# Kernel optimization log

Measured on AMD Instinct MI355X. Metric: run time of the kernel, lower is better.

The kernel has to match this reference:

```python
import jax, jax.numpy as jnp
import numpy as np

B, T, DIM = 1, 4096, 768
H, D = 6, 128  # num_heads, head_dim
ATTN_SCALE = 0.12
EPS = 1.1920929e-07  # torch fp32 rms_norm default eps


def _rms_norm(x):
    # F.rms_norm over last dim, no learned weight
    return x * jax.lax.rsqrt(jnp.mean(jnp.square(x), axis=-1, keepdims=True) + EPS)


def _rotary_tables(seq_len, head_dim):
    # angular_freq: (1/1024)**linspace(0,1,D//4) concat zeros(D//4) -> length D//2
    af = (1.0 / 1024.0) ** jnp.linspace(0.0, 1.0, head_dim // 4, dtype=jnp.float32)
    af = jnp.concatenate([af, jnp.zeros(head_dim // 4, dtype=jnp.float32)])
    t = jnp.arange(seq_len, dtype=jnp.float32)
    theta = t[:, None] * af[None, :]  # [T, D//2]
    return jnp.cos(theta), jnp.sin(theta)


def _apply_rotary(x_bthd, cos, sin):
    # x: [B,T,H,D]; rotate pairs (x1, x2) = halves of last dim
    x1, x2 = jnp.split(x_bthd.astype(jnp.float32), 2, axis=-1)
    c = cos[None, :, None, :]
    s = sin[None, :, None, :]
    y1 = x1 * c + x2 * s
    y2 = -x1 * s + x2 * c
    return jnp.concatenate([y1, y2], axis=-1).astype(x_bthd.dtype)


def setup_inputs() -> dict:
    key = jax.random.key(0)
    k1, k2, k3, k4, k5 = jax.random.split(key, 5)
    std = 0.5 * DIM ** (-0.5)
    bound = (3.0 ** 0.5) * std
    x = jax.random.normal(k1, (B, T, DIM), dtype=jnp.float32)
    ve = jax.random.normal(k2, (B, T, DIM), dtype=jnp.float32)
    qkv_w = jax.random.uniform(k3, (3, H * D, DIM), dtype=jnp.float32, minval=-bound, maxval=bound)
    lambdas = jnp.array([0.5, 0.5], dtype=jnp.float32)
    # original zero-inits c_proj; use small random weights for a nontrivial output
    c_proj_w = jax.random.uniform(k5, (DIM, H * D), dtype=jnp.float32, minval=-bound, maxval=bound)
    return {"x": x, "ve": ve, "qkv_w": qkv_w, "lambdas": lambdas, "c_proj_w": c_proj_w}


def reference(x, ve, qkv_w, lambdas, c_proj_w):
    Bx, Tx = x.shape[0], x.shape[1]
    # fused QKV: linear with weight [3*hdim, dim] -> [B,T,3*H,D]
    qkv = jnp.einsum('btd,ehd->bteh', x, qkv_w.reshape(3 * H, D, DIM).reshape(3 * H * D, DIM).reshape(3 * H, D, DIM))
    # simpler: flatten weight and reshape output
    w_flat = qkv_w.reshape(3 * H * D, DIM)
    qkv = (x @ w_flat.T).reshape(Bx, Tx, 3 * H, D)
    q, k, v = jnp.split(qkv, 3, axis=2)  # each [B,T,H,D]
    q, k = _rms_norm(q), _rms_norm(k)
    cos, sin = _rotary_tables(Tx, D)
    q, k = _apply_rotary(q, cos, sin), _apply_rotary(k, cos, sin)
    v = lambdas[0] * v + lambdas[1] * ve.reshape(Bx, Tx, H, D)
    # causal attention with non-standard scale
    scores = jnp.einsum('bthd,bshd->bhts', q, k) * ATTN_SCALE  # [B,H,T,T]
    causal = jnp.tril(jnp.ones((Tx, Tx), dtype=bool))
    scores = jnp.where(causal[None, None], scores, -jnp.inf)
    probs = jax.nn.softmax(scores, axis=-1)
    y = jnp.einsum('bhts,bshd->bthd', probs, v).reshape(Bx, Tx, H * D)
    return y @ c_proj_w.T
```

## Files before the change

kernel.cpp:

```cpp
#include <hip/hip_runtime.h>
#include <hip/hip_bf16.h>

using bf16 = __hip_bfloat16;
typedef __attribute__((ext_vector_type(8))) __bf16 bf16x8;
typedef __attribute__((ext_vector_type(4))) float f32x4;

static constexpr int T = 4096, DIM = 768, H = 6, D = 128, N3 = 2304;
static constexpr int PPH = 280;
static constexpr float kEps = 1.1920929e-07f;
static constexpr float kC1 = 0.12f * 1.44269504f;
static constexpr float kTHR = 11.54f;

__device__ __forceinline__ void gll16(const bf16* g, bf16* l) {
  __builtin_amdgcn_global_load_lds((const __attribute__((address_space(1))) void*)g,
                                   (__attribute__((address_space(3))) void*)l, 16, 0, 0);
}

__device__ __forceinline__ int pre_qt(int qt) {
  const int k = qt >> 3, rr = qt & 7;
  return qt + 4 * k * (k - 1) + rr * k;
}

__global__ __launch_bounds__(256) void prep(const float* __restrict__ x,
                                            const float* __restrict__ qkv_w,
                                            const float* __restrict__ cproj,
                                            bf16* __restrict__ xb, bf16* __restrict__ wb,
                                            bf16* __restrict__ cb, float2* __restrict__ tab) {
  const int NBX = T * DIM / 2048, NBW = N3 * DIM / 2048, NBC = DIM * DIM / 2048;
  int b = blockIdx.x;
  const int tid = threadIdx.x;
  if (b < NBX + NBW + NBC) {
    const float* in;
    bf16* out;
    if (b < NBX) { in = x; out = xb; }
    else if (b < NBX + NBW) { in = qkv_w; out = wb; b -= NBX; }
    else { in = cproj; out = cb; b -= NBX + NBW; }
    const int i = (b * 256 + tid) * 8;
    const float4 a = *(const float4*)(in + i);
    const float4 c = *(const float4*)(in + i + 4);
    bf16 t[8] = {(bf16)a.x, (bf16)a.y, (bf16)a.z, (bf16)a.w,
                 (bf16)c.x, (bf16)c.y, (bf16)c.z, (bf16)c.w};
    *(int4*)(out + i) = *(const int4*)t;
  } else {
    b -= NBX + NBW + NBC;
    const int i = b * 256 + tid;
    const int t = i >> 5, j = i & 31;
    const float af = exp2f(-10.f * (float)j * (1.f / 31.f));
    float s, c;
    sincosf((float)t * af, &s, &c);
    tab[i] = make_float2(c, s);
  }
}

__global__ __launch_bounds__(256, 4) void gemm_qkv(const bf16* __restrict__ A,
                                                   const bf16* __restrict__ B,
                                                   const float2* __restrict__ tab,
                                                   const float* __restrict__ ve,
                                                   const float* __restrict__ lam,
                                                   bf16* __restrict__ qb,
                                                   bf16* __restrict__ kb,
                                                   bf16* __restrict__ vt) {
  __shared__ bf16 sh[12288];
  const int tid = threadIdx.x, lane = tid & 63, wid = tid >> 6;
  const int slice = blockIdx.x;
  const int brow = blockIdx.y * 64;
  const int bcol = slice * 128;
  const int wm = (wid >> 1) * 32, wn = (wid & 1) * 64;
  const int r = lane & 15, g = lane >> 4;
  f32x4 acc[2][4] = {};
  const int lrow = lane >> 3;
  const int scol = (lane & 7) * 8;
  const bf16* gA = A + (long)(brow + wid * 16 + lrow) * DIM + scol;
  const bf16* gB = B + (long)(bcol + wid * 32 + lrow) * DIM + scol;
  for (int k0 = 0; k0 < DIM; k0 += 64) {
    __syncthreads();
#pragma unroll
    for (int i = 0; i < 2; ++i)
      gll16(gA + (long)i * 8 * DIM + k0, sh + (wid * 16 + i * 8) * 64);
#pragma unroll
    for (int i = 0; i < 4; ++i)
      gll16(gB + (long)i * 8 * DIM + k0, sh + 4096 + (wid * 32 + i * 8) * 64);
    __syncthreads();
#pragma unroll
    for (int kk = 0; kk < 2; ++kk) {
      bf16x8 af[2], bfr[4];
#pragma unroll
      for (int m = 0; m < 2; ++m)
        af[m] = *(const bf16x8*)(sh + (wm + m * 16 + r) * 64 + kk * 32 + g * 8);
#pragma unroll
      for (int n = 0; n < 4; ++n)
        bfr[n] = *(const bf16x8*)(sh + 4096 + (wn + n * 16 + r) * 64 + kk * 32 + g * 8);
#pragma unroll
      for (int m = 0; m < 2; ++m)
#pragma unroll
        for (int n = 0; n < 4; ++n)
          acc[m][n] = __builtin_amdgcn_mfma_f32_16x16x32_bf16(af[m], bfr[n], acc[m][n], 0, 0, 0);
    }
  }
  __syncthreads();
#pragma unroll
  for (int m = 0; m < 2; ++m)
#pragma unroll
    for (int n = 0; n < 4; ++n)
#pragma unroll
      for (int q = 0; q < 4; ++q)
        sh[(wm + m * 16 + g * 4 + q) * 137 + wn + n * 16 + r] = (bf16)acc[m][n][q];
  __syncthreads();
  const int type = slice / 6, h = slice % 6;
  if (type < 2) {
    const int row = tid >> 2, p0 = (tid & 3) * 16;
    const int t = brow + row;
    float x1[16], x2[16];
    float ss = 0.f;
#pragma unroll
    for (int j = 0; j < 16; ++j) {
      x1[j] = __bfloat162float(sh[row * 137 + p0 + j]);
      x2[j] = __bfloat162float(sh[row * 137 + p0 + 64 + j]);
      ss += x1[j] * x1[j] + x2[j] * x2[j];
    }
    ss += __shfl_xor(ss, 1);
    ss += __shfl_xor(ss, 2);
    const float sc = rsqrtf(ss * (1.f / 128.f) + kEps) * (type == 0 ? kC1 : 1.f);
    bf16 y1[16], y2[16];
#pragma unroll
    for (int j = 0; j < 16; ++j) {
      float c = 1.f, s = 0.f;
      if (p0 + j < 32) { const float2 cs = tab[t * 32 + p0 + j]; c = cs.x; s = cs.y; }
      const float a = x1[j] * sc, b = x2[j] * sc;
      y1[j] = (bf16)(a * c + b * s);
      y2[j] = (bf16)(b * c - a * s);
    }
    bf16* dst = (type == 0 ? qb : kb) + ((long)h * T + t) * D + p0;
    *(int4*)(dst) = *(const int4*)&y1[0];
    *(int4*)(dst + 8) = *(const int4*)&y1[8];
    *(int4*)(dst + 64) = *(const int4*)&y2[0];
    *(int4*)(dst + 72) = *(const int4*)&y2[8];
  } else {
    const float l0 = lam[0], l1 = lam[1];
    const int row = tid >> 2, seg = (tid & 3) * 32;
    const float* vs = ve + (long)(brow + row) * DIM + h * D + seg;
#pragma unroll
    for (int j = 0; j < 32; j += 4) {
      const float4 e = *(const float4*)(vs + j);
      const float ef[4] = {e.x, e.y, e.z, e.w};
#pragma unroll
      for (int u = 0; u < 4; ++u) {
        const int c = seg + j + u;
        sh[row * 137 + c] = (bf16)(l0 * __bfloat162float(sh[row * 137 + c]) + l1 * ef[u]);
      }
    }
    __syncthreads();
    const int d = tid >> 1, half = tid & 1;
    bf16 outr[32];
#pragma unroll
    for (int j = 0; j < 32; ++j) outr[j] = sh[(half * 32 + j) * 137 + d];
    bf16* dst = vt + ((long)h * D + d) * T + brow + half * 32;
#pragma unroll
    for (int c = 0; c < 4; ++c)
      *(int4*)(dst + c * 8) = *(const int4*)&outr[c * 8];
  }
}

template <typename CT>
__global__ __launch_bounds__(256, 4) void gemm_bt(const bf16* __restrict__ A,
                                                  const bf16* __restrict__ B,
                                                  CT* __restrict__ C,
                                                  int M, int N, int K) {
  __shared__ bf16 lA[64][64];
  __shared__ bf16 lB[128][64];
  const int tid = threadIdx.x, lane = tid & 63, wid = tid >> 6;
  const int brow = blockIdx.y * 64, bcol = blockIdx.x * 128;
  const int wm = (wid >> 1) * 32, wn = (wid & 1) * 64;
  const int r = lane & 15, g = lane >> 4;
  f32x4 acc[2][4] = {};
  const int lrow = lane >> 3;
  const int scol = (lane & 7) * 8;
  const bf16* gA = A + (long)(brow + wid * 16 + lrow) * K + scol;
  const bf16* gB = B + (long)(bcol + wid * 32 + lrow) * K + scol;
  for (int k0 = 0; k0 < K; k0 += 64) {
    __syncthreads();
#pragma unroll
    for (int i = 0; i < 2; ++i)
      gll16(gA + (long)i * 8 * K + k0, &lA[wid * 16 + i * 8][0]);
#pragma unroll
    for (int i = 0; i < 4; ++i)
      gll16(gB + (long)i * 8 * K + k0, &lB[wid * 32 + i * 8][0]);
    __syncthreads();
#pragma unroll
    for (int kk = 0; kk < 2; ++kk) {
      bf16x8 af[2], bfr[4];
#pragma unroll
      for (int m = 0; m < 2; ++m)
        af[m] = *(const bf16x8*)&lA[wm + m * 16 + r][kk * 32 + g * 8];
#pragma unroll
      for (int n = 0; n < 4; ++n)
        bfr[n] = *(const bf16x8*)&lB[wn + n * 16 + r][kk * 32 + g * 8];
#pragma unroll
      for (int m = 0; m < 2; ++m)
#pragma unroll
        for (int n = 0; n < 4; ++n)
          acc[m][n] = __builtin_amdgcn_mfma_f32_16x16x32_bf16(af[m], bfr[n], acc[m][n], 0, 0, 0);
    }
  }
  const int crow = brow + wm + g * 4;
  const int ccol = bcol + wn + r;
#pragma unroll
  for (int m = 0; m < 2; ++m)
#pragma unroll
    for (int n = 0; n < 4; ++n)
#pragma unroll
      for (int q = 0; q < 4; ++q)
        C[(long)(crow + m * 16 + q) * N + ccol + n * 16] = (CT)acc[m][n][q];
}

__global__ __launch_bounds__(512, 4) void attn(const bf16* __restrict__ qb,
                                               const bf16* __restrict__ kb,
                                               const bf16* __restrict__ vt,
                                               bf16* __restrict__ po,
                                               float* __restrict__ pm,
                                               float* __restrict__ ps,
                                               bf16* __restrict__ yb) {
  __shared__ bf16 Kl[64][128];
  __shared__ bf16 Vl[128][64];
  __shared__ bf16 Pl[8][16][64];
  const int bid = blockIdx.x;
  const int h = bid % H;
  const int fi = bid / H;
  int s = 31, ci = 0, acc0 = 0;
  for (int ss = 31; ss >= 0; --ss) {
    const int n = (ss >> 2) + 1;
    if (fi < acc0 + n) { s = ss; ci = fi - acc0; break; }
    acc0 += n;
  }
  const int tid = threadIdx.x, lane = tid & 63, w = tid >> 6;
  const int r = lane & 15, g = lane >> 4;
  const int qt = 2 * s + (w >> 2);
  const int wrow = (w & 3) * 16;
  const int ts = ci * 8;
  const int te = min(ts + 8, 2 * s + 2);

  bf16x8 qf[4];
#pragma unroll
  for (int kk = 0; kk < 4; ++kk)
    qf[kk] = *(const bf16x8*)(qb + ((long)h * T + qt * 64 + wrow + r) * D + kk * 32 + g * 8);
  f32x4 o[8] = {};
  float m[4], sl[4];
#pragma unroll
  for (int q = 0; q < 4; ++q) { m[q] = -1e30f; sl[q] = 0.f; }

  auto STAGE = [&](int t) {
    const int kv0 = t * 64;
#pragma unroll
    for (int i = 0; i < 2; ++i) {
      const int seg = w * 2 + i;
      {
        const int lr = seg * 4 + (lane >> 4);
        const int cs = (lane & 15) ^ (lr & 7);
        gll16(kb + ((long)h * T + kv0 + lr) * D + cs * 8,
              (bf16*)&Kl[0][0] + seg * 512);
      }
      {
        const int lr = seg * 8 + (lane >> 3);
        const int cs = (lane & 7) ^ (lr & 7);
        gll16(vt + ((long)h * D + lr) * T + kv0 + cs * 8,
              (bf16*)&Vl[0][0] + seg * 512);
      }
    }
  };

  STAGE(ts);
  __syncthreads();
  for (int tt = ts; tt < te; ++tt) {
    const bool act = (tt <= qt);
    if (act) {
      const bf16* Kb = (const bf16*)&Kl[0][0];
      const bf16* Vb = (const bf16*)&Vl[0][0];
      bf16* Pb = &Pl[w][0][0];
      f32x4 st4[4];
      __builtin_amdgcn_s_setprio(1);
#pragma unroll
      for (int stt = 0; stt < 4; ++stt) {
        f32x4 a = {};
        const int lrk = stt * 16 + r;
#pragma unroll
        for (int kk = 0; kk < 4; ++kk) {
          const bf16x8 kf = *(const bf16x8*)(Kb + lrk * 128 + (((kk * 4 + g) ^ (lrk & 7)) * 8));
          a = __builtin_amdgcn_mfma_f32_16x16x32_bf16(qf[kk], kf, a, 0, 0, 0);
        }
        st4[stt] = a;
      }
      __builtin_amdgcn_s_setprio(0);
      if (tt == qt) {
        const int qgl = qt * 64 + wrow + 4 * g;
#pragma unroll
        for (int stt = 0; stt < 4; ++stt)
#pragma unroll
          for (int q = 0; q < 4; ++q)
            if (tt * 64 + stt * 16 + r > qgl + q) st4[stt][q] = -1e30f;
      }
      float mx[4];
#pragma unroll
      for (int q = 0; q < 4; ++q)
        mx[q] = fmaxf(fmaxf(st4[0][q], st4[1][q]), fmaxf(st4[2][q], st4[3][q]));
      const float dd = fmaxf(fmaxf(mx[0] - m[0], mx[1] - m[1]),
                             fmaxf(mx[2] - m[2], mx[3] - m[3]));
      if (__any(dd > kTHR)) {
#pragma unroll
        for (int off = 1; off < 16; off <<= 1)
#pragma unroll
          for (int q = 0; q < 4; ++q) mx[q] = fmaxf(mx[q], __shfl_xor(mx[q], off));
#pragma unroll
        for (int q = 0; q < 4; ++q) {
          const float nm = fmaxf(m[q], mx[q]);
          const float al = exp2f(m[q] - nm);
          m[q] = nm;
          sl[q] *= al;
#pragma unroll
          for (int nn = 0; nn < 8; ++nn) o[nn][q] *= al;
        }
      }
#pragma unroll
      for (int stt = 0; stt < 4; ++stt)
#pragma unroll
        for (int q = 0; q < 4; ++q)
          st4[stt][q] = exp2f(st4[stt][q] - m[q]);
#pragma unroll
      for (int q = 0; q < 4; ++q)
        sl[q] += (st4[0][q] + st4[1][q]) + (st4[2][q] + st4[3][q]);
#pragma unroll
      for (int stt = 0; stt < 4; ++stt)
#pragma unroll
        for (int q = 0; q < 4; ++q) {
          const int rw = 4 * g + q;
          Pb[rw * 64 + ((stt * 16 + r) ^ ((rw & 7) << 3))] = (bf16)st4[stt][q];
        }
      bf16x8 pf[2];
#pragma unroll
      for (int kk = 0; kk < 2; ++kk)
        pf[kk] = *(const bf16x8*)(Pb + r * 64 + (((kk * 4 + g) ^ (r & 7)) * 8));
      __builtin_amdgcn_s_setprio(1);
#pragma unroll
      for (int nn = 0; nn < 8; ++nn) {
        const int d = nn * 16 + r;
#pragma unroll
        for (int kk = 0; kk < 2; ++kk) {
          const bf16x8 vf = *(const bf16x8*)(Vb + d * 64 + (((kk * 4 + g) ^ (d & 7)) * 8));
          o[nn] = __builtin_amdgcn_mfma_f32_16x16x32_bf16(pf[kk], vf, o[nn], 0, 0, 0);
        }
      }
      __builtin_amdgcn_s_setprio(0);
    }
    if (tt + 1 < te) {
      __syncthreads();
      STAGE(tt + 1);
      __syncthreads();
    }
  }
#pragma unroll
  for (int off = 1; off < 16; off <<= 1)
#pragma unroll
    for (int q = 0; q < 4; ++q) sl[q] += __shfl_xor(sl[q], off);
  const int row0 = wrow + 4 * g;
  if (s < 4) {
#pragma unroll
    for (int nn = 0; nn < 8; ++nn)
#pragma unroll
      for (int q = 0; q < 4; ++q)
        yb[(long)(qt * 64 + row0 + q) * DIM + h * D + nn * 16 + r] = (bf16)(o[nn][q] / sl[q]);
  } else {
    const long part = (long)h * PPH + (pre_qt(qt) - 8) + ci;
    bf16* pob = po + part * 8192;
#pragma unroll
    for (int nn = 0; nn < 8; ++nn)
#pragma unroll
      for (int q = 0; q < 4; ++q)
        pob[(row0 + q) * 128 + nn * 16 + r] = (bf16)o[nn][q];
    if (r == 0) {
#pragma unroll
      for (int q = 0; q < 4; ++q) {
        pm[part * 64 + row0 + q] = m[q];
        ps[part * 64 + row0 + q] = sl[q];
      }
    }
  }
}

__global__ __launch_bounds__(256) void attn_reduce(const bf16* __restrict__ po,
                                                   const float* __restrict__ pm,
                                                   const float* __restrict__ ps,
                                                   bf16* __restrict__ yb) {
  const int qt = 8 + blockIdx.x, h = blockIdx.y;
  const int tid = threadIdx.x;
  const int row = tid >> 2, seg = (tid & 3) * 32;
  const int nch = (qt >> 3) + 1;
  const long base = (long)h * PPH + pre_qt(qt) - 8;
  float mm = -1e30f;
  for (int ci = 0; ci < nch; ++ci) mm = fmaxf(mm, pm[(base + ci) * 64 + row]);
  float den = 0.f;
  for (int ci = 0; ci < nch; ++ci)
    den += ps[(base + ci) * 64 + row] * exp2f(pm[(base + ci) * 64 + row] - mm);
  const float inv = 1.f / den;
  float acc[32] = {};
  for (int ci = 0; ci < nch; ++ci) {
    const float wq = exp2f(pm[(base + ci) * 64 + row] - mm) * inv;
    const bf16* src = po + (base + ci) * 8192 + row * 128 + seg;
#pragma unroll
    for (int j = 0; j < 32; j += 8) {
      const bf16x8 v = *(const bf16x8*)(src + j);
#pragma unroll
      for (int u = 0; u < 8; ++u) acc[j + u] += wq * (float)v[u];
    }
  }
  bf16 outv[32];
#pragma unroll
  for (int j = 0; j < 32; ++j) outv[j] = (bf16)acc[j];
  bf16* dst = yb + (long)(qt * 64 + row) * DIM + h * D + seg;
#pragma unroll
  for (int cc = 0; cc < 4; ++cc)
    *(int4*)(dst + cc * 8) = *(const int4*)&outv[cc * 8];
}

extern "C" void kernel_launch(void* const* d_in, const int* in_sizes, int n_in,
                              void* d_out, int out_size, void* d_ws, size_t ws_size,
                              hipStream_t stream) {
  const float* x     = (const float*)d_in[0];
  const float* ve    = (const float*)d_in[1];
  const float* qkv_w = (const float*)d_in[2];
  const float* lam   = (const float*)d_in[3];
  const float* cproj = (const float*)d_in[4];
  float* out = (float*)d_out;

  bf16* cb  = (bf16*)d_ws;
  bf16* qb  = cb + (long)DIM * DIM;
  bf16* kb  = qb + (long)H * T * D;
  bf16* vt  = kb + (long)H * T * D;
  bf16* yb  = vt + (long)H * T * D;
  float2* tab = (float2*)(yb + (long)T * DIM);
  bf16* xb  = (bf16*)(tab + (long)T * 32);
  bf16* wb  = xb + (long)T * DIM;
  bf16* po  = xb;
  float* pm = (float*)(po + (long)PPH * H * 8192);
  float* ps = pm + (long)PPH * H * 64;

  const int NBX = T * DIM / 2048, NBW = N3 * DIM / 2048, NBC = DIM * DIM / 2048;
  prep<<<dim3(NBX + NBW + NBC + T * 32 / 256), 256, 0, stream>>>(x, qkv_w, cproj, xb, wb, cb, tab);

  gemm_qkv<<<dim3(N3 / 128, T / 64), 256, 0, stream>>>(xb, wb, tab, ve, lam, qb, kb, vt);
  attn<<<dim3(144 * H), 512, 0, stream>>>(qb, kb, vt, po, pm, ps, yb);
  attn_reduce<<<dim3(56, H), 256, 0, stream>>>(po, pm, ps, yb);
  gemm_bt<float><<<dim3(DIM / 128, T / 64), 256, 0, stream>>>(yb, cb, out, T, DIM, DIM);
}
```

Before: 134.8 us.

## Double-buffer attention K/V tiles at 32-key granularity and shrink output GEMM tiles

The attention kernel now stages K/V in 32-key tiles across two LDS buffers, prefetching the next tile before computing the current one. This replaces the previous pattern of two barriers around each synchronous 64-key load, so global loads can overlap MFMA work. The split work per block keeps the same key span (16 half-tiles), and the causal mask and active checks are adjusted for the finer granularity. Separately, the output projection GEMM uses 64x64 tiles instead of 64x128, which doubles the number of blocks and helps the small problem fill the GPU. The smaller K-steps mean more loop iterations and more per-tile softmax overhead.

Measured after the change: 131.9 us. 2.2% less time.

```diff
diff --git a/kernel.cpp b/kernel.cpp
--- a/kernel.cpp
+++ b/kernel.cpp
@@ -167,38 +167,37 @@
                                                   CT* __restrict__ C,
                                                   int M, int N, int K) {
   __shared__ bf16 lA[64][64];
-  __shared__ bf16 lB[128][64];
+  __shared__ bf16 lB[64][64];
   const int tid = threadIdx.x, lane = tid & 63, wid = tid >> 6;
-  const int brow = blockIdx.y * 64, bcol = blockIdx.x * 128;
-  const int wm = (wid >> 1) * 32, wn = (wid & 1) * 64;
+  const int brow = blockIdx.y * 64, bcol = blockIdx.x * 64;
+  const int wm = (wid >> 1) * 32, wn = (wid & 1) * 32;
   const int r = lane & 15, g = lane >> 4;
-  f32x4 acc[2][4] = {};
+  f32x4 acc[2][2] = {};
   const int lrow = lane >> 3;
   const int scol = (lane & 7) * 8;
   const bf16* gA = A + (long)(brow + wid * 16 + lrow) * K + scol;
-  const bf16* gB = B + (long)(bcol + wid * 32 + lrow) * K + scol;
+  const bf16* gB = B + (long)(bcol + wid * 16 + lrow) * K + scol;
   for (int k0 = 0; k0 < K; k0 += 64) {
     __syncthreads();
 #pragma unroll
-    for (int i = 0; i < 2; ++i)
+    for (int i = 0; i < 2; ++i) {
       gll16(gA + (long)i * 8 * K + k0, &lA[wid * 16 + i * 8][0]);
-#pragma unroll
-    for (int i = 0; i < 4; ++i)
-      gll16(gB + (long)i * 8 * K + k0, &lB[wid * 32 + i * 8][0]);
+      gll16(gB + (long)i * 8 * K + k0, &lB[wid * 16 + i * 8][0]);
+    }
     __syncthreads();
 #pragma unroll
     for (int kk = 0; kk < 2; ++kk) {
-      bf16x8 af[2], bfr[4];
+      bf16x8 af[2], bfr[2];
 #pragma unroll
       for (int m = 0; m < 2; ++m)
         af[m] = *(const bf16x8*)&lA[wm + m * 16 + r][kk * 32 + g * 8];
 #pragma unroll
-      for (int n = 0; n < 4; ++n)
+      for (int n = 0; n < 2; ++n)
         bfr[n] = *(const bf16x8*)&lB[wn + n * 16 + r][kk * 32 + g * 8];
 #pragma unroll
       for (int m = 0; m < 2; ++m)
 #pragma unroll
-        for (int n = 0; n < 4; ++n)
+        for (int n = 0; n < 2; ++n)
           acc[m][n] = __builtin_amdgcn_mfma_f32_16x16x32_bf16(af[m], bfr[n], acc[m][n], 0, 0, 0);
     }
   }
@@ -207,7 +206,7 @@
 #pragma unroll
   for (int m = 0; m < 2; ++m)
 #pragma unroll
-    for (int n = 0; n < 4; ++n)
+    for (int n = 0; n < 2; ++n)
 #pragma unroll
       for (int q = 0; q < 4; ++q)
         C[(long)(crow + m * 16 + q) * N + ccol + n * 16] = (CT)acc[m][n][q];
@@ -220,9 +219,9 @@
                                                float* __restrict__ pm,
                                                float* __restrict__ ps,
                                                bf16* __restrict__ yb) {
-  __shared__ bf16 Kl[64][128];
-  __shared__ bf16 Vl[128][64];
-  __shared__ bf16 Pl[8][16][64];
+  __shared__ bf16 Kl[2][32][128];
+  __shared__ bf16 Vl[2][128][32];
+  __shared__ bf16 Pl[8][16][32];
   const int bid = blockIdx.x;
   const int h = bid % H;
   const int fi = bid / H;
@@ -236,8 +235,8 @@
   const int r = lane & 15, g = lane >> 4;
   const int qt = 2 * s + (w >> 2);
   const int wrow = (w & 3) * 16;
-  const int ts = ci * 8;
-  const int te = min(ts + 8, 2 * s + 2);
+  const int ts = ci * 16;
+  const int te = min(ts + 16, 4 * s + 4);
 
   bf16x8 qf[4];
 #pragma unroll
@@ -248,38 +247,36 @@
 #pragma unroll
   for (int q = 0; q < 4; ++q) { m[q] = -1e30f; sl[q] = 0.f; }
 
-  auto STAGE = [&](int t) {
-    const int kv0 = t * 64;
-#pragma unroll
-    for (int i = 0; i < 2; ++i) {
-      const int seg = w * 2 + i;
-      {
-        const int lr = seg * 4 + (lane >> 4);
-        const int cs = (lane & 15) ^ (lr & 7);
-        gll16(kb + ((long)h * T + kv0 + lr) * D + cs * 8,
-              (bf16*)&Kl[0][0] + seg * 512);
-      }
-      {
-        const int lr = seg * 8 + (lane >> 3);
-        const int cs = (lane & 7) ^ (lr & 7);
-        gll16(vt + ((long)h * D + lr) * T + kv0 + cs * 8,
-              (bf16*)&Vl[0][0] + seg * 512);
-      }
+  auto STAGE = [&](int buf, int t) {
+    const int kv0 = t * 32;
+    {
+      const int lr = w * 4 + (lane >> 4);
+      const int cs = (lane & 15) ^ (lr & 7);
+      gll16(kb + ((long)h * T + kv0 + lr) * D + cs * 8,
+            (bf16*)&Kl[buf][0][0] + w * 512);
+    }
+    {
+      const int lr = w * 16 + (lane >> 2);
+      const int cs = (lane & 3) ^ ((lr >> 1) & 3);
+      gll16(vt + ((long)h * D + lr) * T + kv0 + cs * 8,
+            (bf16*)&Vl[buf][0][0] + w * 512);
     }
   };
 
-  STAGE(ts);
+  STAGE(0, ts);
   __syncthreads();
+  int cur = 0;
   for (int tt = ts; tt < te; ++tt) {
-    const bool act = (tt <= qt);
+    if (tt + 1 < te) STAGE(cur ^ 1, tt + 1);
+    const bool act = (tt <= 2 * qt + 1);
     if (act) {
-      const bf16* Kb = (const bf16*)&Kl[0][0];
-      const bf16* Vb = (const bf16*)&Vl[0][0];
+      const bf16* Kb = (const bf16*)&Kl[cur][0][0];
+      const bf16* Vb = (const bf16*)&Vl[cur][0][0];
       bf16* Pb = &Pl[w][0][0];
-      f32x4 st4[4];
+      f32x4 st2[2];
       __builtin_amdgcn_s_setprio(1);
 #pragma unroll
-      for (int stt = 0; stt < 4; ++stt) {
+      for (int stt = 0; stt < 2; ++stt) {
         f32x4 a = {};
         const int lrk = stt * 16 + r;
 #pragma unroll
@@ -287,21 +284,21 @@
           const bf16x8 kf = *(const bf16x8*)(Kb + lrk * 128 + (((kk * 4 + g) ^ (lrk & 7)) * 8));
           a = __builtin_amdgcn_mfma_f32_16x16x32_bf16(qf[kk], kf, a, 0, 0, 0);
         }
-        st4[stt] = a;
+        st2[stt] = a;
       }
       __builtin_amdgcn_s_setprio(0);
-      if (tt == qt) {
+      if ((tt >> 1) == qt) {
         const int qgl = qt * 64 + wrow + 4 * g;
-#pragma unroll
-        for (int stt = 0; stt < 4; ++stt)
+        const int ct = tt * 32;
+#pragma unroll
+        for (int stt = 0; stt < 2; ++stt)
 #pragma unroll
           for (int q = 0; q < 4; ++q)
-            if (tt * 64 + stt * 16 + r > qgl + q) st4[stt][q] = -1e30f;
+            if (ct + stt * 16 + r > qgl + q) st2[stt][q] = -1e30f;
       }
       float mx[4];
 #pragma unroll
-      for (int q = 0; q < 4; ++q)
-        mx[q] = fmaxf(fmaxf(st4[0][q], st4[1][q]), fmaxf(st4[2][q], st4[3][q]));
+      for (int q = 0; q < 4; ++q) mx[q] = fmaxf(st2[0][q], st2[1][q]);
       const float dd = fmaxf(fmaxf(mx[0] - m[0], mx[1] - m[1]),
                              fmaxf(mx[2] - m[2], mx[3] - m[3]));
       if (__any(dd > kTHR)) {
@@ -320,41 +317,32 @@
         }
       }
 #pragma unroll
-      for (int stt = 0; stt < 4; ++stt)
+      for (int stt = 0; stt < 2; ++stt)
 #pragma unroll
         for (int q = 0; q < 4; ++q)
-          st4[stt][q] = exp2f(st4[stt][q] - m[q]);
-#pragma unroll
-      for (int q = 0; q < 4; ++q)
-        sl[q] += (st4[0][q] + st4[1][q]) + (st4[2][q] + st4[3][q]);
-#pragma unroll
-      for (int stt = 0; stt < 4; ++stt)
+          st2[stt][q] = exp2f(st2[stt][q] - m[q]);
+#pragma unroll
+      for (int q = 0; q < 4; ++q) sl[q] += st2[0][q] + st2[1][q];
+#pragma unroll
+      for (int stt = 0; stt < 2; ++stt)
 #pragma unroll
         for (int q = 0; q < 4; ++q) {
           const int rw = 4 * g + q;
-          Pb[rw * 64 + ((stt * 16 + r) ^ ((rw & 7) << 3))] = (bf16)st4[stt][q];
+          const int c = stt * 16 + r;
+          Pb[rw * 32 + (c ^ (((rw >> 1) & 3) << 3))] = (bf16)st2[stt][q];
         }
-      bf16x8 pf[2];
-#pragma unroll
-      for (int kk = 0; kk < 2; ++kk)
-        pf[kk] = *(const bf16x8*)(Pb + r * 64 + (((kk * 4 + g) ^ (r & 7)) * 8));
+      const bf16x8 pf = *(const bf16x8*)(Pb + r * 32 + ((g ^ ((r >> 1) & 3)) * 8));
       __builtin_amdgcn_s_setprio(1);
 #pragma unroll
       for (int nn = 0; nn < 8; ++nn) {
         const int d = nn * 16 + r;
-#pragma unroll
-        for (int kk = 0; kk < 2; ++kk) {
-          const bf16x8 vf = *(const bf16x8*)(Vb + d * 64 + (((kk * 4 + g) ^ (d & 7)) * 8));
-          o[nn] = __builtin_amdgcn_mfma_f32_16x16x32_bf16(pf[kk], vf, o[nn], 0, 0, 0);
-        }
+        const bf16x8 vf = *(const bf16x8*)(Vb + d * 32 + ((g ^ ((d >> 1) & 3)) * 8));
+        o[nn] = __builtin_amdgcn_mfma_f32_16x16x32_bf16(pf, vf, o[nn], 0, 0, 0);
       }
       __builtin_amdgcn_s_setprio(0);
     }
-    if (tt + 1 < te) {
-      __syncthreads();
-      STAGE(tt + 1);
-      __syncthreads();
-    }
+    __syncthreads();
+    cur ^= 1;
   }
 #pragma unroll
   for (int off = 1; off < 16; off <<= 1)
@@ -448,5 +436,5 @@
   gemm_qkv<<<dim3(N3 / 128, T / 64), 256, 0, stream>>>(xb, wb, tab, ve, lam, qb, kb, vt);
   attn<<<dim3(144 * H), 512, 0, stream>>>(qb, kb, vt, po, pm, ps, yb);
   attn_reduce<<<dim3(56, H), 256, 0, stream>>>(po, pm, ps, yb);
-  gemm_bt<float><<<dim3(DIM / 128, T / 64), 256, 0, stream>>>(yb, cb, out, T, DIM, DIM);
-}
+  gemm_bt<float><<<dim3(DIM / 64, T / 64), 256, 0, stream>>>(yb, cb, out, T, DIM, DIM);
+}
```
